# Optimization experiments

Hardware: AMD Instinct MI355X
Metric: run time of the kernel (lower is better)

The kernel has to match this reference:

```python
import jax, jax.numpy as jnp
import numpy as np

B, T, D_LAT = 128, 256, 256
N_HIDDEN = 1024
H_SMALL = N_HIDDEN // 2  # 512: lstm1/lstm2 hidden size
H_BIG = N_HIDDEN         # 1024: lstm3 hidden size


def _p(key, shape, scale=0.05):
    return (jax.random.normal(key, shape, dtype=jnp.float32) * scale)


def setup_inputs() -> dict:
    key = jax.random.key(0)
    ks = jax.random.split(key, 16)
    return {
        "X": jax.random.normal(ks[0], (B, T, D_LAT), dtype=jnp.float32),
        # LSTMCell 1: input D_LAT -> hidden H_SMALL (torch layout: [4H, in])
        "W_ih1": _p(ks[1], (4 * H_SMALL, D_LAT)),
        "W_hh1": _p(ks[2], (4 * H_SMALL, H_SMALL)),
        "b_ih1": _p(ks[3], (4 * H_SMALL,)),
        "b_hh1": _p(ks[4], (4 * H_SMALL,)),
        # LSTMCell 2: H_SMALL -> H_SMALL
        "W_ih2": _p(ks[5], (4 * H_SMALL, H_SMALL)),
        "W_hh2": _p(ks[6], (4 * H_SMALL, H_SMALL)),
        "b_ih2": _p(ks[7], (4 * H_SMALL,)),
        "b_hh2": _p(ks[8], (4 * H_SMALL,)),
        # LSTMCell 3: H_SMALL -> H_BIG
        "W_ih3": _p(ks[9], (4 * H_BIG, H_SMALL)),
        "W_hh3": _p(ks[10], (4 * H_BIG, H_BIG)),
        "b_ih3": _p(ks[11], (4 * H_BIG,)),
        "b_hh3": _p(ks[12], (4 * H_BIG,)),
        # Linear: H_BIG -> D_LAT (torch layout: [out, in])
        "W_lin": _p(ks[13], (D_LAT, H_BIG)),
        "b_lin": _p(ks[14], (D_LAT,)),
    }


def _lstm_cell(x, h, c, W_ih, W_hh, b_ih, b_hh):
    # torch.nn.LSTMCell gate order: i, f, g, o
    gates = x @ W_ih.T + b_ih + h @ W_hh.T + b_hh  # [B, 4H]
    i, f, g, o = jnp.split(gates, 4, axis=-1)
    c_new = jax.nn.sigmoid(f) * c + jax.nn.sigmoid(i) * jnp.tanh(g)
    h_new = jax.nn.sigmoid(o) * jnp.tanh(c_new)
    return h_new, c_new


def reference(X, W_ih1, W_hh1, b_ih1, b_hh1,
              W_ih2, W_hh2, b_ih2, b_hh2,
              W_ih3, W_hh3, b_ih3, b_hh3,
              W_lin, b_lin):
    n = X.shape[0]
    z_s = jnp.zeros((n, H_SMALL), dtype=X.dtype)
    z_b = jnp.zeros((n, H_BIG), dtype=X.dtype)
    init = (z_s, z_s, z_s, z_s, z_b, z_b)

    def step(carry, x_t):
        h1, c1, h2, c2, h3, c3 = carry
        h1, c1 = _lstm_cell(x_t, h1, c1, W_ih1, W_hh1, b_ih1, b_hh1)
        h2, c2 = _lstm_cell(h1, h2, c2, W_ih2, W_hh2, b_ih2, b_hh2)
        h3, c3 = _lstm_cell(h2, h3, c3, W_ih3, W_hh3, b_ih3, b_hh3)
        out = h3 @ W_lin.T + b_lin  # [B, D_LAT]
        return (h1, c1, h2, c2, h3, c3), out

    xs = jnp.swapaxes(X, 0, 1)  # [T, B, D_LAT]
    _, outputs = jax.lax.scan(step, init, xs)
    return outputs  # [T, B, D_LAT] == torch.stack(outputs) with future=0
```

## Files before the change

### kernel.cpp

```cpp
#include <hip/hip_runtime.h>
#include <stdint.h>

#define NWG 208
#define NPHASE 259

typedef __attribute__((ext_vector_type(8))) short short8;
typedef __attribute__((ext_vector_type(4))) float floatx4;
typedef __attribute__((ext_vector_type(4))) unsigned int uintx4;

static constexpr int Bb = 128, Tt = 256, Dl = 256, Hs = 512, Hb = 1024;

static constexpr size_t OFF_FLAGS = 0;
static constexpr size_t OFF_B1  = 1024;
static constexpr size_t OFF_B2  = OFF_B1 + 2048*4;
static constexpr size_t OFF_B3  = OFF_B2 + 2048*4;
static constexpr size_t OFF_BL  = OFF_B3 + 4096*4;
static constexpr size_t OFF_W1  = OFF_BL + 1024;
static constexpr size_t OFF_W2  = OFF_W1 + (size_t)2048*768*2;
static constexpr size_t OFF_W3  = OFF_W2 + (size_t)2048*1024*2;
static constexpr size_t OFF_WL  = OFF_W3 + (size_t)4096*1536*2;
static constexpr size_t FIXED_END = OFF_WL + (size_t)256*1024*2;

template<int D> struct Lay {
  static constexpr size_t H1  = FIXED_END;
  static constexpr size_t H2  = H1 + (size_t)D*Bb*Hs*2;
  static constexpr size_t H3  = H2 + (size_t)D*Bb*Hs*2;
  static constexpr size_t XB  = H3 + (size_t)D*Bb*Hb*2;
  static constexpr size_t END = XB + (size_t)D*Bb*Dl*2;
};

__device__ __forceinline__ unsigned short f2bf(float f) {
  unsigned int u = __float_as_uint(f);
  unsigned int r = (u + 0x7fffu + ((u >> 16) & 1u)) >> 16;
  return (unsigned short)r;
}
__device__ __forceinline__ float sigm(float x) { return 1.f/(1.f + __expf(-x)); }
__device__ __forceinline__ float tanh_f(float x) {
  x = fminf(fmaxf(x, -15.f), 15.f);
  float e = __expf(-2.f*x);
  return (1.f - e)/(1.f + e);
}

__device__ __forceinline__ size_t blk_off(int row, int u) {
  return ((size_t)(u >> 5)*8 + (row >> 4))*512 + (size_t)((u & 31) >> 3)*128
       + (size_t)(row & 15)*8 + (u & 7);
}

__device__ __forceinline__ void st_short_cg(unsigned short* p, unsigned int v) {
  asm volatile("global_store_short %0, %1, off sc0 sc1" :: "v"(p), "v"(v) : "memory");
}
__device__ __forceinline__ void st_dword_cg(void* p, unsigned int v) {
  asm volatile("global_store_dword %0, %1, off sc0 sc1" :: "v"(p), "v"(v) : "memory");
}
__device__ __forceinline__ void st_b128_cg(void* p, uintx4 v) {
  asm volatile("global_store_dwordx4 %0, %1, off sc0 sc1" :: "v"(p), "v"(v) : "memory");
}
__device__ __forceinline__ void waitcnt_vm0() {
  asm volatile("s_waitcnt vmcnt(0)" ::: "memory");
}

template<int D>
__global__ void lstm_init(
    const float* __restrict__ X,
    const float* __restrict__ Wih1, const float* __restrict__ Whh1,
    const float* __restrict__ bih1, const float* __restrict__ bhh1,
    const float* __restrict__ Wih2, const float* __restrict__ Whh2,
    const float* __restrict__ bih2, const float* __restrict__ bhh2,
    const float* __restrict__ Wih3, const float* __restrict__ Whh3,
    const float* __restrict__ bih3, const float* __restrict__ bhh3,
    const float* __restrict__ Wlin, const float* __restrict__ blin,
    unsigned char* __restrict__ ws)
{
  size_t i0 = (size_t)blockIdx.x*blockDim.x + threadIdx.x;
  size_t np = (size_t)gridDim.x*blockDim.x;

  unsigned int* fl = (unsigned int*)(ws + OFF_FLAGS);
  for (size_t i = i0; i < 256; i += np) fl[i] = (i < NWG) ? 0u : 0xFFFFFFFFu;

  float* b1 = (float*)(ws + OFF_B1);
  float* b2 = (float*)(ws + OFF_B2);
  float* b3 = (float*)(ws + OFF_B3);
  float* bl = (float*)(ws + OFF_BL);
  for (size_t i = i0; i < 2048; i += np) b1[i] = bih1[i] + bhh1[i];
  for (size_t i = i0; i < 2048; i += np) b2[i] = bih2[i] + bhh2[i];
  for (size_t i = i0; i < 4096; i += np) b3[i] = bih3[i] + bhh3[i];
  for (size_t i = i0; i < 256;  i += np) bl[i] = blin[i];

  unsigned short* w1 = (unsigned short*)(ws + OFF_W1);
  unsigned short* w2 = (unsigned short*)(ws + OFF_W2);
  unsigned short* w3 = (unsigned short*)(ws + OFF_W3);
  unsigned short* wl = (unsigned short*)(ws + OFF_WL);
  for (size_t i = i0; i < (size_t)2048*768; i += np) {
    size_t r = i/768, k = i - r*768;
    float v = (k < 256) ? Wih1[r*256 + k] : Whh1[r*512 + (k - 256)];
    w1[i] = f2bf(v);
  }
  for (size_t i = i0; i < (size_t)2048*1024; i += np) {
    size_t r = i >> 10, k = i & 1023;
    float v = (k < 512) ? Wih2[r*512 + k] : Whh2[r*512 + (k - 512)];
    w2[i] = f2bf(v);
  }
  for (size_t i = i0; i < (size_t)4096*1536; i += np) {
    size_t r = i/1536, k = i - r*1536;
    float v = (k < 512) ? Wih3[r*512 + k] : Whh3[r*1024 + (k - 512)];
    w3[i] = f2bf(v);
  }
  for (size_t i = i0; i < (size_t)256*1024; i += np) wl[i] = f2bf(Wlin[i]);

  unsigned short* rings = (unsigned short*)(ws + Lay<D>::H1);
  const size_t nring = (size_t)D*Bb*Hs + (size_t)D*Bb*Hs + (size_t)D*Bb*Hb;
  for (size_t i = i0; i < nring; i += np) rings[i] = 0;

  unsigned short* xb0 = (unsigned short*)(ws + Lay<D>::XB);
  for (size_t i = i0; i < (size_t)Bb*Dl; i += np) {
    size_t b = i >> 8, d = i & 255;
    xb0[blk_off((int)b, (int)d)] = f2bf(X[(b*(size_t)Tt + 0)*Dl + d]);
  }
}

template<int TYPE>
__device__ __forceinline__ void layer_phase(
    const unsigned short* __restrict__ segA,
    const unsigned short* __restrict__ segB,
    unsigned short* __restrict__ hout,
    const unsigned char* __restrict__ smem,
    const float* __restrict__ bias_r,
    float (&creg)[4][2][4],
    int U0, int wv, int lane)
{
  constexpr int K    = (TYPE==0 ? 768 : TYPE==1 ? 1024 : 1536);
  constexpr int KB1  = (TYPE==0 ? 256 : 512);
  constexpr int MF   = (TYPE==2 ? 2 : 4);
  constexpr int NCH  = K/128;
  const int l15 = lane & 15;
  const int klo = (lane >> 4) << 3;
  const int g   = l15 >> 2;
  const int mbase = (TYPE==2 ? wv*32 : (wv&1)*64);
  const int nfb   = (TYPE==2 ? 0 : (wv>>1)*2);

  const size_t lof = (size_t)(lane >> 4)*128 + (size_t)l15*8;
  const unsigned short* pa[MF];
  const unsigned short* pb[MF];
  #pragma unroll
  for (int mf = 0; mf < MF; ++mf) {
    const size_t rb = (size_t)((mbase >> 4) + mf)*512;
    pa[mf] = segA + rb + lof;
    pb[mf] = segB + rb + lof;
  }
  int rowbyte[2], xr[2];
  #pragma unroll
  for (int nf = 0; nf < 2; ++nf) {
    const int rp = (nfb + nf)*16 + l15;
    rowbyte[nf] = rp*(K*2);
    xr[nf] = (rp & 7) << 4;
  }
  const int klobyte = klo*2;

  floatx4 acc[MF][2];
  #pragma unroll
  for (int mf = 0; mf < MF; ++mf)
    #pragma unroll
    for (int nf = 0; nf < 2; ++nf) {
      float bv = bias_r[nf];
      floatx4 b4 = {bv, bv, bv, bv};
      acc[mf][nf] = b4;
    }

  short8 A0[4][MF], A1[4][MF];
  auto LOADC = [&](int c, short8 (&A)[4][MF]) {
    #pragma unroll
    for (int ks = 0; ks < 4; ++ks) {
      const int kb = c*128 + ks*32;
      #pragma unroll
      for (int mf = 0; mf < MF; ++mf) {
        const unsigned short* p = (kb < KB1)
            ? pa[mf] + (size_t)(kb >> 5)*4096
            : pb[mf] + (size_t)((kb - KB1) >> 5)*4096;
        A[ks][mf] = *(const short8*)p;
      }
    }
  };
  auto MM = [&](int c, short8 (&A)[4][MF]) {
    #pragma unroll
    for (int ks = 0; ks < 4; ++ks) {
      const int kb = c*128 + ks*32;
      short8 bf[2];
      #pragma unroll
      for (int nf = 0; nf < 2; ++nf)
        bf[nf] = *(const short8*)(smem + rowbyte[nf] + ((kb*2 + klobyte) ^ xr[nf]));
      #pragma unroll
      for (int mf = 0; mf < MF; ++mf)
        #pragma unroll
        for (int nf = 0; nf < 2; ++nf)
          acc[mf][nf] = __builtin_amdgcn_mfma_f32_16x16x32_bf16(A[ks][mf], bf[nf], acc[mf][nf], 0, 0, 0);
    }
  };

  LOADC(0, A0);
  #pragma unroll 1
  for (int ch = 0; ch < NCH; ch += 2) {
    LOADC(ch + 1, A1);
    MM(ch, A0);
    if (ch + 2 < NCH) LOADC(ch + 2, A0);
    MM(ch + 1, A1);
  }

  #pragma unroll
  for (int nf = 0; nf < 2; ++nf) {
    const int u = U0 + (nfb + nf)*4 + (l15 & 3);
    #pragma unroll
    for (int mf = 0; mf < MF; ++mf) {
      float h4[4];
      #pragma unroll
      for (int j = 0; j < 4; ++j) {
        float s0  = acc[mf][nf][j];
        float s4  = __shfl_xor(s0, 4);
        float s8  = __shfl_xor(s0, 8);
        float s12 = __shfl_xor(s0, 12);
        float iv = (g==0)?s0 :(g==1)?s4 :(g==2)?s8 :s12;
        float fv = (g==0)?s4 :(g==1)?s0 :(g==2)?s12:s8;
        float gv = (g==0)?s8 :(g==1)?s12:(g==2)?s0 :s4;
        float ov = (g==0)?s12:(g==1)?s8 :(g==2)?s4 :s0;
        float c  = sigm(fv)*creg[mf][nf][j] + sigm(iv)*tanh_f(gv);
        creg[mf][nf][j] = c;
        h4[j] = sigm(ov)*tanh_f(c);
      }
      float hs = (g==0)?h4[0]:(g==1)?h4[1]:(g==2)?h4[2]:h4[3];
      const int row = mbase + mf*16 + ((lane >> 4) << 2) + g;
      st_short_cg(hout + blk_off(row, u), (unsigned int)f2bf(hs));
    }
  }
}

template<int D>
__global__ void __launch_bounds__(256, 1)
lstm_persist(const float* __restrict__ X, float* __restrict__ out,
             unsigned char* __restrict__ ws)
{
  extern __shared__ unsigned char smem[];

  __builtin_amdgcn_fence(__ATOMIC_ACQUIRE, "agent");

  const int tid  = threadIdx.x;
  const int lane = tid & 63;
  const int wv   = tid >> 6;
  const int wg   = blockIdx.x;
  const int l15  = lane & 15;

  unsigned int* flags = (unsigned int*)(ws + OFF_FLAGS);
  const float* bias1 = (const float*)(ws + OFF_B1);
  const float* bias2 = (const float*)(ws + OFF_B2);
  const float* bias3 = (const float*)(ws + OFF_B3);
  const float* biasl = (const float*)(ws + OFF_BL);
  const unsigned short* W1 = (const unsigned short*)(ws + OFF_W1);
  const unsigned short* W2 = (const unsigned short*)(ws + OFF_W2);
  const unsigned short* W3 = (const unsigned short*)(ws + OFF_W3);
  const unsigned short* WL = (const unsigned short*)(ws + OFF_WL);
  unsigned short* h1r = (unsigned short*)(ws + Lay<D>::H1);
  unsigned short* h2r = (unsigned short*)(ws + Lay<D>::H2);
  unsigned short* h3r = (unsigned short*)(ws + Lay<D>::H3);
  unsigned short* Xb  = (unsigned short*)(ws + Lay<D>::XB);

  auto slot = [](int t) -> size_t { return (size_t)(t & (D - 1)); };
  const size_t HSs = (size_t)Bb*Hs, HBs = (size_t)Bb*Hb, XBs = (size_t)Bb*Dl;

  int type, U0 = 0, osec = 0, K = 0, WROWS = 0, HGATE = 0;
  const unsigned short* Wg = nullptr; const float* biasp = nullptr;
  if (wg < 32)        { type = 0; U0 = wg*16;        Wg = W1; biasp = bias1; K = 768;  WROWS = 64; HGATE = 512; }
  else if (wg < 64)   { type = 1; U0 = (wg-32)*16;   Wg = W2; biasp = bias2; K = 1024; WROWS = 64; HGATE = 512; }
  else if (wg < 192)  { type = 2; U0 = (wg-64)*8;    Wg = W3; biasp = bias3; K = 1536; WROWS = 32; HGATE = 1024; }
  else                { type = 3; osec = (wg-192)*16; Wg = WL; K = 1024; WROWS = 16; }

  {
    const int rowchunks = K >> 3;
    for (int idx = tid; idx < WROWS*rowchunks; idx += 256) {
      const int rp = idx / rowchunks, kc = idx - rp*rowchunks;
      int R;
      if (type == 3) R = osec + rp;
      else {
        const int c = rp & 15;
        R = (c >> 2)*HGATE + U0 + (rp >> 4)*4 + (c & 3);
      }
      uintx4 v = *(const uintx4*)(Wg + (size_t)R*K + kc*8);
      const int db = rp*(K*2) + ((kc*16) ^ ((rp & 7) << 4));
      *(uintx4*)(smem + db) = v;
    }
  }

  float bias_r[2] = {0.f, 0.f};
  if (type < 3) {
    const int g   = l15 >> 2;
    const int nfb = (type == 2 ? 0 : (wv >> 1)*2);
    #pragma unroll
    for (int nf = 0; nf < 2; ++nf) {
      const int u = U0 + (nfb + nf)*4 + (l15 & 3);
      bias_r[nf] = biasp[g*HGATE + u];
    }
  } else {
    bias_r[0] = biasl[osec + l15];
  }

  float creg[4][2][4];
  #pragma unroll
  for (int a = 0; a < 4; ++a)
    #pragma unroll
    for (int b = 0; b < 2; ++b)
      #pragma unroll
      for (int c = 0; c < 4; ++c) creg[a][b][c] = 0.f;

  __syncthreads();

  for (int p = 0; p < NPHASE; ++p) {
    if (type == 0) {
      const int t = p;
      if (t < Tt)
        layer_phase<0>(Xb + slot(t)*XBs,
                       h1r + slot(t-1)*HSs,
                       h1r + slot(t)*HSs,
                       smem, bias_r, creg, U0, wv, lane);
    } else if (type == 1) {
      const int t = p - 1;
      if (t >= 0 && t < Tt)
        layer_phase<1>(h1r + slot(t)*HSs,
                       h2r + slot(t-1)*HSs,
                       h2r + slot(t)*HSs,
                       smem, bias_r, creg, U0, wv, lane);
    } else if (type == 2) {
      const int t = p - 2;
      if (t >= 0 && t < Tt)
        layer_phase<2>(h2r + slot(t)*HSs,
                       h3r + slot(t-1)*HBs,
                       h3r + slot(t)*HBs,
                       smem, bias_r, creg, U0, wv, lane);
    } else {
      if (p + 1 < Tt) {
        const int tx = p + 1;
        const int j = wg - 192;
        const int i = tid*8;
        const int row = j*8 + (i >> 8);
        const int d = i & 255;
        const float* xp = X + ((size_t)row*Tt + tx)*Dl + d;
        float4 f0 = *(const float4*)xp;
        float4 f1 = *(const float4*)(xp + 4);
        uintx4 pk;
        pk[0] = (unsigned int)f2bf(f0.x) | ((unsigned int)f2bf(f0.y) << 16);
        pk[1] = (unsigned int)f2bf(f0.z) | ((unsigned int)f2bf(f0.w) << 16);
        pk[2] = (unsigned int)f2bf(f1.x) | ((unsigned int)f2bf(f1.y) << 16);
        pk[3] = (unsigned int)f2bf(f1.z) | ((unsigned int)f2bf(f1.w) << 16);
        st_b128_cg(Xb + slot(tx)*XBs + blk_off(row, d), pk);
      }
      const int to = p - 3;
      if (to >= 0 && to < Tt) {
        const unsigned short* hA = h3r + slot(to)*HBs;
        const size_t lof = (size_t)(lane >> 4)*128 + (size_t)l15*8;
        const unsigned short* pa[2];
        #pragma unroll
        for (int mf = 0; mf < 2; ++mf)
          pa[mf] = hA + (size_t)((wv*32 + mf*16) >> 4)*512 + lof;
        const int rowbyte = l15*2048;
        const int xr = (l15 & 7) << 4;
        const int klobyte = ((lane >> 4) << 3)*2;
        floatx4 oacc[2];
        {
          floatx4 b4 = {bias_r[0], bias_r[0], bias_r[0], bias_r[0]};
          oacc[0] = b4; oacc[1] = b4;
        }
        short8 A0[4][2], A1[4][2];
        auto HLOAD = [&](int c, short8 (&A)[4][2]) {
          #pragma unroll
          for (int ks = 0; ks < 4; ++ks)
            #pragma unroll
            for (int mf = 0; mf < 2; ++mf)
              A[ks][mf] = *(const short8*)(pa[mf] + (size_t)(c*4 + ks)*4096);
        };
        auto HMM = [&](int c, short8 (&A)[4][2]) {
          #pragma unroll
          for (int ks = 0; ks < 4; ++ks) {
            const int kb = c*128 + ks*32;
            short8 bw = *(const short8*)(smem + rowbyte + ((kb*2 + klobyte) ^ xr));
            #pragma unroll
            for (int mf = 0; mf < 2; ++mf)
              oacc[mf] = __builtin_amdgcn_mfma_f32_16x16x32_bf16(A[ks][mf], bw, oacc[mf], 0, 0, 0);
          }
        };
        HLOAD(0, A0);
        #pragma unroll 1
        for (int ch = 0; ch < 8; ch += 2) {
          HLOAD(ch + 1, A1);
          HMM(ch, A0);
          if (ch + 2 < 8) HLOAD(ch + 2, A0);
          HMM(ch + 1, A1);
        }
        const int col = osec + l15;
        #pragma unroll
        for (int mf = 0; mf < 2; ++mf) {
          const int b0 = wv*32 + mf*16 + ((lane >> 4) << 2);
          #pragma unroll
          for (int j = 0; j < 4; ++j)
            st_dword_cg(out + ((size_t)to*Bb + b0 + j)*Dl + col,
                        __float_as_uint(oacc[mf][j]));
        }
      }
    }

    if (p < NPHASE - 1) {
      waitcnt_vm0();
      __syncthreads();
      const unsigned int tgt = (unsigned int)(p + 1);
      if (tid == 0) st_dword_cg(flags + wg, tgt);
      if (tid < 64) {
        uintx4 f;
        for (;;) {
          asm volatile("global_load_dwordx4 %0, %1, off sc0 sc1\n\t"
                       "s_waitcnt vmcnt(0)"
                       : "=v"(f) : "v"(flags + lane*4) : "memory");
          if (f[0] >= tgt && f[1] >= tgt && f[2] >= tgt && f[3] >= tgt) break;
          __builtin_amdgcn_s_sleep(4);
        }
      }
      __syncthreads();
      if (D == 2 || (p & 7) == 7)
        __builtin_amdgcn_fence(__ATOMIC_ACQUIRE, "agent");
    }
  }
}

extern "C" void kernel_launch(void* const* d_in, const int* in_sizes, int n_in,
                              void* d_out, int out_size, void* d_ws, size_t ws_size,
                              hipStream_t stream)
{
  const float* X    = (const float*)d_in[0];
  const float* Wih1 = (const float*)d_in[1];
  const float* Whh1 = (const float*)d_in[2];
  const float* bih1 = (const float*)d_in[3];
  const float* bhh1 = (const float*)d_in[4];
  const float* Wih2 = (const float*)d_in[5];
  const float* Whh2 = (const float*)d_in[6];
  const float* bih2 = (const float*)d_in[7];
  const float* bhh2 = (const float*)d_in[8];
  const float* Wih3 = (const float*)d_in[9];
  const float* Whh3 = (const float*)d_in[10];
  const float* bih3 = (const float*)d_in[11];
  const float* bhh3 = (const float*)d_in[12];
  const float* Wlin = (const float*)d_in[13];
  const float* blin = (const float*)d_in[14];
  unsigned char* ws = (unsigned char*)d_ws;

  if (ws_size >= Lay<8>::END) {
    lstm_init<8><<<2048, 256, 0, stream>>>(X, Wih1, Whh1, bih1, bhh1,
                                           Wih2, Whh2, bih2, bhh2,
                                           Wih3, Whh3, bih3, bhh3,
                                           Wlin, blin, ws);
    lstm_persist<8><<<NWG, 256, 131072, stream>>>(X, (float*)d_out, ws);
  } else if (ws_size >= Lay<2>::END) {
    lstm_init<2><<<2048, 256, 0, stream>>>(X, Wih1, Whh1, bih1, bhh1,
                                           Wih2, Whh2, bih2, bhh2,
                                           Wih3, Whh3, bih3, bhh3,
                                           Wlin, blin, ws);
    lstm_persist<2><<<NWG, 256, 131072, stream>>>(X, (float*)d_out, ws);
  }
}
```

Baseline: 3.951 ms.

## Stage h outputs in LDS for 128-bit stores and triple-buffer A loads

Each lane's hidden-state value used to be written to global memory as its own 2-byte store. Those values are now gathered into a small LDS staging area and, after a block barrier, written out as 16-byte vector stores. The A-operand load pipeline changes from double buffering to a fully unrolled triple buffer, with a larger per-chunk k-depth for layer 3. The aim is to cut the number of small coherent global stores on the critical recurrent path and to hide load latency better, at the cost of an extra __syncthreads, 4 KB more LDS, and higher register pressure from the third buffer.

```diff
diff --git a/kernel.cpp b/kernel.cpp
--- a/kernel.cpp
+++ b/kernel.cpp
@@ -29,6 +29,9 @@
   static constexpr size_t END = XB + (size_t)D*Bb*Dl*2;
 };
 
+static constexpr int SMEM_BYTES = 135168;
+static constexpr int STG_OFF    = 131072;
+
 __device__ __forceinline__ unsigned short f2bf(float f) {
   unsigned int u = __float_as_uint(f);
   unsigned int r = (u + 0x7fffu + ((u >> 16) & 1u)) >> 16;
@@ -40,14 +43,9 @@
   float e = __expf(-2.f*x);
   return (1.f - e)/(1.f + e);
 }
-
 __device__ __forceinline__ size_t blk_off(int row, int u) {
   return ((size_t)(u >> 5)*8 + (row >> 4))*512 + (size_t)((u & 31) >> 3)*128
        + (size_t)(row & 15)*8 + (u & 7);
-}
-
-__device__ __forceinline__ void st_short_cg(unsigned short* p, unsigned int v) {
-  asm volatile("global_store_short %0, %1, off sc0 sc1" :: "v"(p), "v"(v) : "memory");
 }
 __device__ __forceinline__ void st_dword_cg(void* p, unsigned int v) {
   asm volatile("global_store_dword %0, %1, off sc0 sc1" :: "v"(p), "v"(v) : "memory");
@@ -123,15 +121,16 @@
     const unsigned short* __restrict__ segA,
     const unsigned short* __restrict__ segB,
     unsigned short* __restrict__ hout,
-    const unsigned char* __restrict__ smem,
+    unsigned char* __restrict__ smem,
     const float* __restrict__ bias_r,
     float (&creg)[4][2][4],
-    int U0, int wv, int lane)
+    int U0, int wv, int lane, int tid)
 {
   constexpr int K    = (TYPE==0 ? 768 : TYPE==1 ? 1024 : 1536);
   constexpr int KB1  = (TYPE==0 ? 256 : 512);
   constexpr int MF   = (TYPE==2 ? 2 : 4);
-  constexpr int NCH  = K/128;
+  constexpr int CKS  = (TYPE==2 ? 8 : 4);
+  constexpr int NCH  = K/(32*CKS);
   const int l15 = lane & 15;
   const int klo = (lane >> 4) << 3;
   const int g   = l15 >> 2;
@@ -166,24 +165,24 @@
       acc[mf][nf] = b4;
     }
 
-  short8 A0[4][MF], A1[4][MF];
-  auto LOADC = [&](int c, short8 (&A)[4][MF]) {
-    #pragma unroll
-    for (int ks = 0; ks < 4; ++ks) {
-      const int kb = c*128 + ks*32;
+  short8 A[3][CKS][MF];
+  auto LOADC = [&](int c, int buf) {
+    #pragma unroll
+    for (int ks = 0; ks < CKS; ++ks) {
+      const int kb = (c*CKS + ks)*32;
       #pragma unroll
       for (int mf = 0; mf < MF; ++mf) {
         const unsigned short* p = (kb < KB1)
             ? pa[mf] + (size_t)(kb >> 5)*4096
             : pb[mf] + (size_t)((kb - KB1) >> 5)*4096;
-        A[ks][mf] = *(const short8*)p;
+        A[buf][ks][mf] = *(const short8*)p;
       }
     }
   };
-  auto MM = [&](int c, short8 (&A)[4][MF]) {
-    #pragma unroll
-    for (int ks = 0; ks < 4; ++ks) {
-      const int kb = c*128 + ks*32;
+  auto MM = [&](int c, int buf) {
+    #pragma unroll
+    for (int ks = 0; ks < CKS; ++ks) {
+      const int kb = (c*CKS + ks)*32;
       short8 bf[2];
       #pragma unroll
       for (int nf = 0; nf < 2; ++nf)
@@ -192,19 +191,20 @@
       for (int mf = 0; mf < MF; ++mf)
         #pragma unroll
         for (int nf = 0; nf < 2; ++nf)
-          acc[mf][nf] = __builtin_amdgcn_mfma_f32_16x16x32_bf16(A[ks][mf], bf[nf], acc[mf][nf], 0, 0, 0);
+          acc[mf][nf] = __builtin_amdgcn_mfma_f32_16x16x32_bf16(A[buf][ks][mf], bf[nf], acc[mf][nf], 0, 0, 0);
     }
   };
 
-  LOADC(0, A0);
-  #pragma unroll 1
-  for (int ch = 0; ch < NCH; ch += 2) {
-    LOADC(ch + 1, A1);
-    MM(ch, A0);
-    if (ch + 2 < NCH) LOADC(ch + 2, A0);
-    MM(ch + 1, A1);
-  }
-
+  LOADC(0, 0);
+  LOADC(1, 1);
+  #pragma unroll
+  for (int ch = 0; ch < NCH; ++ch) {
+    if (ch + 2 < NCH) LOADC(ch + 2, (ch + 2) % 3);
+    MM(ch, ch % 3);
+  }
+
+  unsigned short* stg = (unsigned short*)(smem + STG_OFF);
+  const int a = (U0 & 31) >> 3;
   #pragma unroll
   for (int nf = 0; nf < 2; ++nf) {
     const int u = U0 + (nfb + nf)*4 + (l15 & 3);
@@ -227,8 +227,24 @@
       }
       float hs = (g==0)?h4[0]:(g==1)?h4[1]:(g==2)?h4[2]:h4[3];
       const int row = mbase + mf*16 + ((lane >> 4) << 2) + g;
-      st_short_cg(hout + blk_off(row, u), (unsigned int)f2bf(hs));
-    }
+      const int c2  = (TYPE==2) ? (row >> 4)
+                                : ((row >> 4)*2 + (((u & 31) >> 3) - a));
+      stg[c2*128 + (row & 15)*8 + (u & 7)] = f2bf(hs);
+    }
+  }
+  __syncthreads();
+
+  const size_t gbase = (size_t)(U0 >> 5)*4096;
+  if (TYPE == 2) {
+    if (tid < 128) {
+      const int c2 = tid >> 4, w = tid & 15;
+      short8 v = *(const short8*)(stg + c2*128 + w*8);
+      st_b128_cg(hout + gbase + (size_t)c2*512 + (size_t)a*128 + w*8, *(uintx4*)&v);
+    }
+  } else {
+    const int c2 = tid >> 4, w = tid & 15;
+    short8 v = *(const short8*)(stg + c2*128 + w*8);
+    st_b128_cg(hout + gbase + (size_t)(c2 >> 1)*512 + (size_t)(a + (c2 & 1))*128 + w*8, *(uintx4*)&v);
   }
 }
 
@@ -317,21 +333,21 @@
         layer_phase<0>(Xb + slot(t)*XBs,
                        h1r + slot(t-1)*HSs,
                        h1r + slot(t)*HSs,
-                       smem, bias_r, creg, U0, wv, lane);
+                       smem, bias_r, creg, U0, wv, lane, tid);
     } else if (type == 1) {
       const int t = p - 1;
       if (t >= 0 && t < Tt)
         layer_phase<1>(h1r + slot(t)*HSs,
                        h2r + slot(t-1)*HSs,
                        h2r + slot(t)*HSs,
-                       smem, bias_r, creg, U0, wv, lane);
+                       smem, bias_r, creg, U0, wv, lane, tid);
     } else if (type == 2) {
       const int t = p - 2;
       if (t >= 0 && t < Tt)
         layer_phase<2>(h2r + slot(t)*HSs,
                        h3r + slot(t-1)*HBs,
                        h3r + slot(t)*HBs,
-                       smem, bias_r, creg, U0, wv, lane);
+                       smem, bias_r, creg, U0, wv, lane, tid);
     } else {
       if (p + 1 < Tt) {
         const int tx = p + 1;
@@ -451,12 +467,12 @@
                                            Wih2, Whh2, bih2, bhh2,
                                            Wih3, Whh3, bih3, bhh3,
                                            Wlin, blin, ws);
-    lstm_persist<8><<<NWG, 256, 131072, stream>>>(X, (float*)d_out, ws);
+    lstm_persist<8><<<NWG, 256, SMEM_BYTES, stream>>>(X, (float*)d_out, ws);
   } else if (ws_size >= Lay<2>::END) {
     lstm_init<2><<<2048, 256, 0, stream>>>(X, Wih1, Whh1, bih1, bhh1,
                                            Wih2, Whh2, bih2, bhh2,
                                            Wih3, Whh3, bih3, bhh3,
                                            Wlin, blin, ws);
-    lstm_persist<2><<<NWG, 256, 131072, stream>>>(X, (float*)d_out, ws);
-  }
-}
+    lstm_persist<2><<<NWG, 256, SMEM_BYTES, stream>>>(X, (float*)d_out, ws);
+  }
+}
```

Measured after the change: 4.602 ms. 16.5% more time.
